# Kernel optimization log

Hardware: AMD Instinct MI355X
Metric: run time of the kernel (lower is better)

## Reference

```python
import jax, jax.numpy as jnp
import numpy as np

# Module hyper-parameters (match init_kwargs)
H = 8          # num_heads
F = 32         # attention_filters
HF = H * F     # 256, equals input channels C
RY, RX = 2, 2  # spatial_radius
PH, PW = 2 * RY + 1, 2 * RX + 1
S = PH * PW    # 25 neighbor offsets


def setup_inputs() -> dict:
    key = jax.random.key(0)
    ks = jax.random.split(key, 6)
    B, Y, X, C = 8, 128, 128, 256
    x = jax.random.normal(ks[0], (B, Y, X, C), dtype=jnp.float32)
    sc = 0.02
    Wq = jax.random.normal(ks[1], (C, HF), dtype=jnp.float32) * sc
    Wk = jax.random.normal(ks[2], (C, HF), dtype=jnp.float32) * sc
    Wv = jax.random.normal(ks[3], (C, HF), dtype=jnp.float32) * sc
    Wout = jax.random.normal(ks[4], (HF, C), dtype=jnp.float32) * sc
    pos_emb = jax.random.normal(ks[5], (S, HF), dtype=jnp.float32) * sc
    return {"x": x, "Wq": Wq, "Wk": Wk, "Wv": Wv, "Wout": Wout, "pos_emb": pos_emb}


def _centers(n, r):
    # clipped patch-center coordinate for each position
    c = jnp.arange(n)
    return jnp.clip(c, r, n - r - 1)


def reference(x, Wq, Wk, Wv, Wout, pos_emb):
    B, Y, X, C = x.shape
    dtype = x.dtype
    # 1x1 conv projections == channel matmuls
    Q = jnp.einsum('byxc,cf->byxf', x, Wq)
    K = jnp.einsum('byxc,cf->byxf', x, Wk)
    V = jnp.einsum('byxc,cf->byxf', x, Wv)

    # query spatial positional embedding (relative position to clipped center)
    yc = _centers(Y, RY)
    xc = _centers(X, RX)
    y_rel = jnp.arange(Y) - yc + RY          # [Y]
    x_rel = jnp.arange(X) - xc + RX          # [X]
    q_idx = y_rel[:, None] * PW + x_rel[None, :]  # [Y, X]
    Q = Q + pos_emb[q_idx]                   # [B,Y,X,HF]
    Q = Q.reshape(B, Y, X, H, F)

    scale = jnp.asarray(1.0 / np.sqrt(F), dtype)

    offsets = [(dy, dx) for dy in range(-RY, RY + 1) for dx in range(-RX, RX + 1)]

    # pass 1: per-offset scores (loop over fixed 25-neighborhood, rest vectorized)
    scores = []
    for s_idx, (dy, dx) in enumerate(offsets):
        ny = jnp.clip(yc + dy, 0, Y - 1)     # [Y]
        nx = jnp.clip(xc + dx, 0, X - 1)     # [X]
        Kn = K[:, ny][:, :, nx] + pos_emb[s_idx]        # [B,Y,X,HF]
        Kn = Kn.reshape(B, Y, X, H, F)
        scores.append(jnp.einsum('byxhf,byxhf->byxh', Q, Kn) * scale)
    scores = jnp.stack(scores, axis=-1)      # [B,Y,X,H,S]
    weights = jax.nn.softmax(scores, axis=-1)

    # pass 2: weighted value accumulation
    out_acc = jnp.zeros((B, Y, X, H, F), dtype=dtype)
    for s_idx, (dy, dx) in enumerate(offsets):
        ny = jnp.clip(yc + dy, 0, Y - 1)
        nx = jnp.clip(xc + dx, 0, X - 1)
        Vn = V[:, ny][:, :, nx].reshape(B, Y, X, H, F)
        out_acc = out_acc + weights[..., s_idx, None] * Vn

    out_acc = out_acc.reshape(B, Y, X, HF)
    out = jnp.einsum('byxf,fc->byxc', out_acc, Wout)
    return out
```

## Files before the change

### kernel.cpp

```cpp
#include <hip/hip_runtime.h>

#define DEVI __device__ __forceinline__

typedef short v8s __attribute__((ext_vector_type(8)));
typedef float v4f __attribute__((ext_vector_type(4)));
typedef _Float16 h2v __attribute__((ext_vector_type(2)));
typedef __fp16 fp16x2 __attribute__((ext_vector_type(2)));
typedef unsigned short u16;

typedef __attribute__((address_space(3))) unsigned int lds_u32;
typedef const __attribute__((address_space(1))) unsigned int glb_u32;

DEVI float bf2f(short s) {
  union { unsigned u; float f; } cv;
  cv.u = ((unsigned)(u16)s) << 16;
  return cv.f;
}
DEVI short f2bf(float f) {
  union { float f; unsigned u; } cv; cv.f = f;
  unsigned u = cv.u;
  return (short)((u + 0x7FFFu + ((u >> 16) & 1u)) >> 16);
}
DEVI unsigned cvtpk(float lo, float hi) {
  unsigned r;
  asm("v_cvt_pk_bf16_f32 %0, %1, %2" : "=v"(r) : "v"(lo), "v"(hi));
  return r;
}
DEVI unsigned pkh(float a, float b) {
  union { fp16x2 h; unsigned u; } cv;
  cv.h = __builtin_amdgcn_cvt_pkrtz(a, b);
  return cv.u;
}
DEVI float fdot2u(unsigned a, unsigned b, float c) {
  union { unsigned u; h2v h; } ca, cb; ca.u = a; cb.u = b;
  return __builtin_amdgcn_fdot2(ca.h, cb.h, c, false);
}
DEVI float h2lo(unsigned u) { union { unsigned u; h2v h; } c; c.u = u; return (float)c.h.x; }
DEVI float h2hi(unsigned u) { union { unsigned u; h2v h; } c; c.u = u; return (float)c.h.y; }
DEVI void gld16(const void* g, void* l) {
  __builtin_amdgcn_global_load_lds((glb_u32*)g, (lds_u32*)l, 16, 0, 0);
}

__global__ void prep_weights(const float* __restrict__ Wq, const float* __restrict__ Wk,
                             const float* __restrict__ Wv, const float* __restrict__ Wout,
                             short* __restrict__ WcT, short* __restrict__ WoT) {
  int n = blockIdx.x;
  int k = threadIdx.x;
  float v;
  if (n < 256)      v = Wq[k * 256 + n];
  else if (n < 512) v = Wk[k * 256 + (n - 256)];
  else              v = Wv[k * 256 + (n - 512)];
  WcT[n * 256 + k] = f2bf(v);
  if (n < 256) WoT[n * 256 + k] = f2bf(Wout[k * 256 + n]);
}

__global__ void x_cast(const float* __restrict__ x, short* __restrict__ xb) {
  for (size_t gidx = (size_t)blockIdx.x * 256 + threadIdx.x; gidx < 4194304;
       gidx += (size_t)4096 * 256) {
    const float4* src = reinterpret_cast<const float4*>(x + gidx * 8);
    float4 a = src[0], c = src[1];
    v8s pk;
    pk[0] = f2bf(a.x); pk[1] = f2bf(a.y); pk[2] = f2bf(a.z); pk[3] = f2bf(a.w);
    pk[4] = f2bf(c.x); pk[5] = f2bf(c.y); pk[6] = f2bf(c.z); pk[7] = f2bf(c.w);
    *reinterpret_cast<v8s*>(xb + gidx * 8) = pk;
  }
}

__launch_bounds__(512, 2)
__global__ void proj_gemm(const short* __restrict__ xb, const short* __restrict__ WcT,
                          const float* __restrict__ pos_emb,
                          short* __restrict__ Qb, short* __restrict__ Kb,
                          short* __restrict__ Vb) {
  __shared__ short As[2][256 * 64];
  __shared__ short Bs[2][256 * 64];
  const int t = threadIdx.x;
  const int bi = blockIdx.x;
  const int xcd = bi & 7;
  const int j = bi >> 3;
  const int mtl = j / 3, nt = j % 3;
  const int mt = xcd * 64 + mtl;
  const int m0 = mt * 256, n0 = nt * 256;
  const int wave = t >> 6, lane = t & 63;
  const int wm = (wave >> 2) * 128, wn = (wave & 3) * 64;
  const int lr = lane & 15, g = lane >> 4;

  const int ro = lane >> 3;
  const int colb = ((lane & 7) * 16) ^ (ro << 4);
  const char* aSrc0 = reinterpret_cast<const char*>(xb + (size_t)(m0 + ro) * 256) + colb;
  const char* bSrc0 = reinterpret_cast<const char*>(WcT + (size_t)(n0 + ro) * 256) + colb;

  auto stage = [&](int buf, int ks) {
#pragma unroll
    for (int c = 0; c < 4; ++c) {
      int cc = wave * 4 + c;
      gld16(aSrc0 + (size_t)cc * 8 * 512 + ks * 128, (char*)As[buf] + cc * 1024);
      gld16(bSrc0 + (size_t)cc * 8 * 512 + ks * 128, (char*)Bs[buf] + cc * 1024);
    }
  };

  v4f acc[8][4];
#pragma unroll
  for (int i = 0; i < 8; ++i)
#pragma unroll
    for (int jj = 0; jj < 4; ++jj) acc[i][jj] = (v4f){0.f, 0.f, 0.f, 0.f};

  stage(0, 0);
  __syncthreads();

#pragma unroll 1
  for (int s = 0; s < 4; ++s) {
    const int buf = s & 1;
    if (s < 3) stage(buf ^ 1, s + 1);

    const char* aB = (const char*)As[buf];
    const char* bB = (const char*)Bs[buf];
#pragma unroll
    for (int kk = 0; kk < 2; ++kk) {
      v8s bfr[4];
#pragma unroll
      for (int jj = 0; jj < 4; ++jj) {
        int rn = wn + jj * 16 + lr;
        bfr[jj] = *reinterpret_cast<const v8s*>(
            bB + ((rn * 128 + kk * 64 + g * 16) ^ ((rn & 7) << 4)));
      }
#pragma unroll
      for (int i = 0; i < 8; ++i) {
        int row = wm + i * 16 + lr;
        v8s af = *reinterpret_cast<const v8s*>(
            aB + ((row * 128 + kk * 64 + g * 16) ^ ((row & 7) << 4)));
#pragma unroll
        for (int jj = 0; jj < 4; ++jj)
          acc[i][jj] = __builtin_amdgcn_mfma_f32_16x16x32_bf16(bfr[jj], af, acc[i][jj], 0, 0, 0);
      }
    }
    __syncthreads();
  }

  short* dst = (nt == 0) ? Qb : (nt == 1) ? Kb : Vb;
#pragma unroll
  for (int i = 0; i < 8; ++i) {
    int p = m0 + wm + i * 16 + lr;
    int qi = 0;
    if (nt == 0) {
      int yy = (p >> 7) & 127, xx = p & 127;
      qi = (yy - min(max(yy, 2), 125) + 2) * 5 + (xx - min(max(xx, 2), 125) + 2);
    }
#pragma unroll
    for (int jj = 0; jj < 4; ++jj) {
      int nb = wn + jj * 16 + g * 4;
      v4f a = acc[i][jj];
      if (nt == 0) {
        float4 pe4 = *reinterpret_cast<const float4*>(pos_emb + qi * 256 + nb);
        a[0] += pe4.x; a[1] += pe4.y; a[2] += pe4.z; a[3] += pe4.w;
      }
      uint2 pk;
      if (nt == 2) {
        pk.x = cvtpk(a[0], a[1]);
        pk.y = cvtpk(a[2], a[3]);
      } else {
        pk.x = pkh(a[0], a[1]);
        pk.y = pkh(a[2], a[3]);
      }
      *reinterpret_cast<uint2*>(dst + (size_t)p * 256 + nb) = pk;
    }
  }
}

__launch_bounds__(256, 4)
__global__ void attn_kernel(const short* __restrict__ Qb, const short* __restrict__ Kb,
                            const short* __restrict__ Vb, const float* __restrict__ pos_emb,
                            short* __restrict__ ACC) {
  __shared__ float pe[25 * 256];
  for (int i = threadIdx.x; i < 1600; i += 256) {
    float4 vv = reinterpret_cast<const float4*>(pos_emb)[i];
    int w = i * 4;
    int f = w & 255;
    int dst = (w & ~255) + (f ^ ((f >> 5) << 2));
    *reinterpret_cast<float4*>(pe + dst) = vv;
  }

  const int t = threadIdx.x;
  const int half = t & 1, h = (t >> 1) & 7, pl = t >> 4;
  const int id = blockIdx.x;
  const int b = id & 7;
  const int local = id >> 3;
  const int bx = local & 31, by = local >> 5;
  const int xx = bx * 4 + (pl & 3);
  const int yy = by * 4 + (pl >> 2);
  const int yc = min(max(yy, 2), 125), xc = min(max(xx, 2), 125);
  const int fo = h * 32 + half * 16;
  const int hx4 = h << 2;
  const size_t pbase = ((size_t)((b * 128 + yy) * 128 + xx)) * 256 + fo;
  const size_t cbase = ((size_t)((b * 128 + yc) * 128 + xc)) * 256 + fo;
  const float SCALE2 = 0.17677669529663689f * 1.4426950408889634f;

  uint4 qA = *reinterpret_cast<const uint4*>(Qb + pbase);
  uint4 qB = *reinterpret_cast<const uint4*>(Qb + pbase + 8);
  float q[16];
  q[0] = h2lo(qA.x); q[1] = h2hi(qA.x); q[2] = h2lo(qA.y); q[3] = h2hi(qA.y);
  q[4] = h2lo(qA.z); q[5] = h2hi(qA.z); q[6] = h2lo(qA.w); q[7] = h2hi(qA.w);
  q[8] = h2lo(qB.x); q[9] = h2hi(qB.x); q[10] = h2lo(qB.y); q[11] = h2hi(qB.y);
  q[12] = h2lo(qB.z); q[13] = h2hi(qB.z); q[14] = h2lo(qB.w); q[15] = h2hi(qB.w);
  __syncthreads();

  float l = 0.f;
  float oa[16];
#pragma unroll
  for (int f = 0; f < 16; ++f) oa[f] = 0.f;

  const short* kb = Kb + cbase;
  const short* vb = Vb + cbase;
  const float* pb = pe + h * 32;
  const int j0 = (half * 16) ^ hx4;
  const int j1 = (half * 16 + 4) ^ hx4;
  const int j2 = (half * 16 + 8) ^ hx4;
  const int j3 = (half * 16 + 12) ^ hx4;

  uint4 kn0, kn1;
  v8s vn0, vn1;
  {
    const short* kp = kb + (-2 * 128 - 2) * 256;
    const short* vp = vb + (-2 * 128 - 2) * 256;
    kn0 = *reinterpret_cast<const uint4*>(kp);
    kn1 = *reinterpret_cast<const uint4*>(kp + 8);
    vn0 = *reinterpret_cast<const v8s*>(vp);
    vn1 = *reinterpret_cast<const v8s*>(vp + 8);
  }

#pragma unroll 1
  for (int dy = -2; dy <= 2; ++dy) {
    const float* prow = pb + ((dy + 2) * 5) * 256;
#pragma unroll 1
    for (int dx = -2; dx <= 2; ++dx) {
      uint4 k0 = kn0, k1 = kn1;
      v8s v0 = vn0, v1 = vn1;
      int ndx = dx + 1, ndy = dy;
      if (ndx > 2) { ndx = -2; ndy = dy + 1; }
      if (ndy <= 2) {
        const short* kp2 = kb + (ndy * 128 + ndx) * 256;
        const short* vp2 = vb + (ndy * 128 + ndx) * 256;
        kn0 = *reinterpret_cast<const uint4*>(kp2);
        kn1 = *reinterpret_cast<const uint4*>(kp2 + 8);
        vn0 = *reinterpret_cast<const v8s*>(vp2);
        vn1 = *reinterpret_cast<const v8s*>(vp2 + 8);
      }
      const float* pp = prow + (dx + 2) * 256;
      float4 p0 = *reinterpret_cast<const float4*>(pp + j0);
      float4 p1 = *reinterpret_cast<const float4*>(pp + j1);
      float4 p2 = *reinterpret_cast<const float4*>(pp + j2);
      float4 p3 = *reinterpret_cast<const float4*>(pp + j3);

      float d0 = 0.f, d1 = 0.f, d2 = 0.f, d3 = 0.f;
      d0 = fdot2u(qA.x, k0.x, d0); d1 = fdot2u(qA.y, k0.y, d1);
      d2 = fdot2u(qA.z, k0.z, d2); d3 = fdot2u(qA.w, k0.w, d3);
      d0 = fdot2u(qB.x, k1.x, d0); d1 = fdot2u(qB.y, k1.y, d1);
      d2 = fdot2u(qB.z, k1.z, d2); d3 = fdot2u(qB.w, k1.w, d3);

      d0 = fmaf(q[0], p0.x, d0); d0 = fmaf(q[1], p0.y, d0);
      d0 = fmaf(q[2], p0.z, d0); d0 = fmaf(q[3], p0.w, d0);
      d1 = fmaf(q[4], p1.x, d1); d1 = fmaf(q[5], p1.y, d1);
      d1 = fmaf(q[6], p1.z, d1); d1 = fmaf(q[7], p1.w, d1);
      d2 = fmaf(q[8], p2.x, d2); d2 = fmaf(q[9], p2.y, d2);
      d2 = fmaf(q[10], p2.z, d2); d2 = fmaf(q[11], p2.w, d2);
      d3 = fmaf(q[12], p3.x, d3); d3 = fmaf(q[13], p3.y, d3);
      d3 = fmaf(q[14], p3.z, d3); d3 = fmaf(q[15], p3.w, d3);

      float part = ((d0 + d1) + (d2 + d3)) * SCALE2;
      float full = part + __shfl_xor(part, 1);
      float w = exp2f(full);
      l += w;
#pragma unroll
      for (int e = 0; e < 8; ++e) oa[e] = fmaf(w, bf2f(v0[e]), oa[e]);
#pragma unroll
      for (int e = 0; e < 8; ++e) oa[8 + e] = fmaf(w, bf2f(v1[e]), oa[8 + e]);
    }
  }

  float inv = 1.f / l;
  uint4 o0, o1;
  o0.x = cvtpk(oa[0] * inv, oa[1] * inv);
  o0.y = cvtpk(oa[2] * inv, oa[3] * inv);
  o0.z = cvtpk(oa[4] * inv, oa[5] * inv);
  o0.w = cvtpk(oa[6] * inv, oa[7] * inv);
  o1.x = cvtpk(oa[8] * inv, oa[9] * inv);
  o1.y = cvtpk(oa[10] * inv, oa[11] * inv);
  o1.z = cvtpk(oa[12] * inv, oa[13] * inv);
  o1.w = cvtpk(oa[14] * inv, oa[15] * inv);
  *reinterpret_cast<uint4*>(ACC + pbase) = o0;
  *reinterpret_cast<uint4*>(ACC + pbase + 8) = o1;
}

__launch_bounds__(512, 2)
__global__ void out_gemm(const short* __restrict__ A, const short* __restrict__ WoT,
                         float* __restrict__ out) {
  __shared__ short As[2][256 * 64];
  __shared__ short Bs[2][256 * 64];
  const int t = threadIdx.x;
  const int bi = blockIdx.x;
  const int xcd = bi & 7;
  const int mt = xcd * 64 + (bi >> 3);
  const int m0 = mt * 256;
  const int wave = t >> 6, lane = t & 63;
  const int wm = (wave >> 2) * 128, wn = (wave & 3) * 64;
  const int lr = lane & 15, g = lane >> 4;

  const int ro = lane >> 3;
  const int colb = ((lane & 7) * 16) ^ (ro << 4);
  const char* aSrc0 = reinterpret_cast<const char*>(A + (size_t)(m0 + ro) * 256) + colb;
  const char* bSrc0 = reinterpret_cast<const char*>(WoT + (size_t)ro * 256) + colb;

  auto stage = [&](int buf, int ks) {
#pragma unroll
    for (int c = 0; c < 4; ++c) {
      int cc = wave * 4 + c;
      gld16(aSrc0 + (size_t)cc * 8 * 512 + ks * 128, (char*)As[buf] + cc * 1024);
      gld16(bSrc0 + (size_t)cc * 8 * 512 + ks * 128, (char*)Bs[buf] + cc * 1024);
    }
  };

  v4f acc[8][4];
#pragma unroll
  for (int i = 0; i < 8; ++i)
#pragma unroll
    for (int jj = 0; jj < 4; ++jj) acc[i][jj] = (v4f){0.f, 0.f, 0.f, 0.f};

  stage(0, 0);
  __syncthreads();

#pragma unroll 1
  for (int s = 0; s < 4; ++s) {
    const int buf = s & 1;
    if (s < 3) stage(buf ^ 1, s + 1);

    const char* aB = (const char*)As[buf];
    const char* bB = (const char*)Bs[buf];
#pragma unroll
    for (int kk = 0; kk < 2; ++kk) {
      v8s bfr[4];
#pragma unroll
      for (int jj = 0; jj < 4; ++jj) {
        int rn = wn + jj * 16 + lr;
        bfr[jj] = *reinterpret_cast<const v8s*>(
            bB + ((rn * 128 + kk * 64 + g * 16) ^ ((rn & 7) << 4)));
      }
#pragma unroll
      for (int i = 0; i < 8; ++i) {
        int row = wm + i * 16 + lr;
        v8s af = *reinterpret_cast<const v8s*>(
            aB + ((row * 128 + kk * 64 + g * 16) ^ ((row & 7) << 4)));
#pragma unroll
        for (int jj = 0; jj < 4; ++jj)
          acc[i][jj] = __builtin_amdgcn_mfma_f32_16x16x32_bf16(bfr[jj], af, acc[i][jj], 0, 0, 0);
      }
    }
    __syncthreads();
  }

#pragma unroll
  for (int i = 0; i < 8; ++i) {
    int p = m0 + wm + i * 16 + lr;
#pragma unroll
    for (int jj = 0; jj < 4; ++jj) {
      int nb = wn + jj * 16 + g * 4;
      float4 o;
      o.x = acc[i][jj][0]; o.y = acc[i][jj][1];
      o.z = acc[i][jj][2]; o.w = acc[i][jj][3];
      *reinterpret_cast<float4*>(out + (size_t)p * 256 + nb) = o;
    }
  }
}

extern "C" void kernel_launch(void* const* d_in, const int* in_sizes, int n_in,
                              void* d_out, int out_size, void* d_ws, size_t ws_size,
                              hipStream_t stream) {
  const float* x       = (const float*)d_in[0];
  const float* Wq      = (const float*)d_in[1];
  const float* Wk      = (const float*)d_in[2];
  const float* Wv      = (const float*)d_in[3];
  const float* Wout    = (const float*)d_in[4];
  const float* pos_emb = (const float*)d_in[5];
  float* out = (float*)d_out;

  char* ws = (char*)d_ws;
  short* WcT  = (short*)ws;
  short* WoT  = (short*)(ws + 393216);
  short* Qb   = (short*)(ws + 524288);
  short* Kb   = Qb + (size_t)131072 * 256;
  short* Vb   = Kb + (size_t)131072 * 256;
  short* ACCb = Vb + (size_t)131072 * 256;
  short* xb   = ACCb;

  prep_weights<<<768, 256, 0, stream>>>(Wq, Wk, Wv, Wout, WcT, WoT);
  x_cast<<<4096, 256, 0, stream>>>(x, xb);
  proj_gemm<<<1536, 512, 0, stream>>>(xb, WcT, pos_emb, Qb, Kb, Vb);
  attn_kernel<<<8192, 256, 0, stream>>>(Qb, Kb, Vb, pos_emb, ACCb);
  out_gemm<<<512, 512, 0, stream>>>(ACCb, WoT, out);
}
```

Baseline: 357.7 us.

## Rework attention kernel: fp16 V/pos-emb, packed half2 accumulation, one thread per head

```diff
diff --git a/kernel.cpp b/kernel.cpp
--- a/kernel.cpp
+++ b/kernel.cpp
@@ -1,4 +1,5 @@
 #include <hip/hip_runtime.h>
+#include <hip/hip_fp16.h>
 
 #define DEVI __device__ __forceinline__
 
@@ -35,8 +36,7 @@
   union { unsigned u; h2v h; } ca, cb; ca.u = a; cb.u = b;
   return __builtin_amdgcn_fdot2(ca.h, cb.h, c, false);
 }
-DEVI float h2lo(unsigned u) { union { unsigned u; h2v h; } c; c.u = u; return (float)c.h.x; }
-DEVI float h2hi(unsigned u) { union { unsigned u; h2v h; } c; c.u = u; return (float)c.h.y; }
+DEVI __half2 uh2(unsigned u) { union { unsigned u; __half2 h; } c; c.u = u; return c.h; }
 DEVI void gld16(const void* g, void* l) {
   __builtin_amdgcn_global_load_lds((glb_u32*)g, (lds_u32*)l, 16, 0, 0);
 }
@@ -154,140 +154,161 @@
         a[0] += pe4.x; a[1] += pe4.y; a[2] += pe4.z; a[3] += pe4.w;
       }
       uint2 pk;
-      if (nt == 2) {
-        pk.x = cvtpk(a[0], a[1]);
-        pk.y = cvtpk(a[2], a[3]);
-      } else {
-        pk.x = pkh(a[0], a[1]);
-        pk.y = pkh(a[2], a[3]);
-      }
+      pk.x = pkh(a[0], a[1]);
+      pk.y = pkh(a[2], a[3]);
       *reinterpret_cast<uint2*>(dst + (size_t)p * 256 + nb) = pk;
     }
   }
 }
 
-__launch_bounds__(256, 4)
+__launch_bounds__(256, 2)
 __global__ void attn_kernel(const short* __restrict__ Qb, const short* __restrict__ Kb,
                             const short* __restrict__ Vb, const float* __restrict__ pos_emb,
                             short* __restrict__ ACC) {
-  __shared__ float pe[25 * 256];
+  __shared__ __align__(16) unsigned pe16[25 * 128];
   for (int i = threadIdx.x; i < 1600; i += 256) {
     float4 vv = reinterpret_cast<const float4*>(pos_emb)[i];
-    int w = i * 4;
-    int f = w & 255;
-    int dst = (w & ~255) + (f ^ ((f >> 5) << 2));
-    *reinterpret_cast<float4*>(pe + dst) = vv;
+    int s = i >> 6;
+    int jw = (i & 63) * 2;
+    int swz = (jw & ~15) | ((((jw >> 2) ^ (jw >> 5)) & 3) << 2) | (jw & 3);
+    uint2 pk2;
+    pk2.x = pkh(vv.x, vv.y);
+    pk2.y = pkh(vv.z, vv.w);
+    *reinterpret_cast<uint2*>(pe16 + s * 128 + swz) = pk2;
   }
 
   const int t = threadIdx.x;
-  const int half = t & 1, h = (t >> 1) & 7, pl = t >> 4;
+  const int h = t & 7, pl = t >> 3;
   const int id = blockIdx.x;
   const int b = id & 7;
   const int local = id >> 3;
   const int bx = local & 31, by = local >> 5;
   const int xx = bx * 4 + (pl & 3);
-  const int yy = by * 4 + (pl >> 2);
+  const int yy = by * 8 + (pl >> 2);
   const int yc = min(max(yy, 2), 125), xc = min(max(xx, 2), 125);
-  const int fo = h * 32 + half * 16;
-  const int hx4 = h << 2;
+  const int fo = h * 32;
   const size_t pbase = ((size_t)((b * 128 + yy) * 128 + xx)) * 256 + fo;
   const size_t cbase = ((size_t)((b * 128 + yc) * 128 + xc)) * 256 + fo;
   const float SCALE2 = 0.17677669529663689f * 1.4426950408889634f;
 
-  uint4 qA = *reinterpret_cast<const uint4*>(Qb + pbase);
-  uint4 qB = *reinterpret_cast<const uint4*>(Qb + pbase + 8);
-  float q[16];
-  q[0] = h2lo(qA.x); q[1] = h2hi(qA.x); q[2] = h2lo(qA.y); q[3] = h2hi(qA.y);
-  q[4] = h2lo(qA.z); q[5] = h2hi(qA.z); q[6] = h2lo(qA.w); q[7] = h2hi(qA.w);
-  q[8] = h2lo(qB.x); q[9] = h2hi(qB.x); q[10] = h2lo(qB.y); q[11] = h2hi(qB.y);
-  q[12] = h2lo(qB.z); q[13] = h2hi(qB.z); q[14] = h2lo(qB.w); q[15] = h2hi(qB.w);
+  uint4 q0 = *reinterpret_cast<const uint4*>(Qb + pbase);
+  uint4 q1 = *reinterpret_cast<const uint4*>(Qb + pbase + 8);
+  uint4 q2 = *reinterpret_cast<const uint4*>(Qb + pbase + 16);
+  uint4 q3 = *reinterpret_cast<const uint4*>(Qb + pbase + 24);
   __syncthreads();
 
+  const unsigned* peb = pe16 + h * 16;
+  const int hs = (h >> 1) & 3;
+  const int r0 = ((0 ^ hs) & 3) * 4;
+  const int r1 = ((1 ^ hs) & 3) * 4;
+  const int r2 = ((2 ^ hs) & 3) * 4;
+  const int r3 = ((3 ^ hs) & 3) * 4;
+
   float l = 0.f;
-  float oa[16];
-#pragma unroll
-  for (int f = 0; f < 16; ++f) oa[f] = 0.f;
+  __half2 oa[16];
+#pragma unroll
+  for (int j = 0; j < 16; ++j) oa[j] = uh2(0u);
 
   const short* kb = Kb + cbase;
   const short* vb = Vb + cbase;
-  const float* pb = pe + h * 32;
-  const int j0 = (half * 16) ^ hx4;
-  const int j1 = (half * 16 + 4) ^ hx4;
-  const int j2 = (half * 16 + 8) ^ hx4;
-  const int j3 = (half * 16 + 12) ^ hx4;
-
-  uint4 kn0, kn1;
-  v8s vn0, vn1;
-  {
-    const short* kp = kb + (-2 * 128 - 2) * 256;
-    const short* vp = vb + (-2 * 128 - 2) * 256;
-    kn0 = *reinterpret_cast<const uint4*>(kp);
-    kn1 = *reinterpret_cast<const uint4*>(kp + 8);
-    vn0 = *reinterpret_cast<const v8s*>(vp);
-    vn1 = *reinterpret_cast<const v8s*>(vp + 8);
-  }
 
 #pragma unroll 1
   for (int dy = -2; dy <= 2; ++dy) {
-    const float* prow = pb + ((dy + 2) * 5) * 256;
-#pragma unroll 1
-    for (int dx = -2; dx <= 2; ++dx) {
-      uint4 k0 = kn0, k1 = kn1;
-      v8s v0 = vn0, v1 = vn1;
-      int ndx = dx + 1, ndy = dy;
-      if (ndx > 2) { ndx = -2; ndy = dy + 1; }
-      if (ndy <= 2) {
-        const short* kp2 = kb + (ndy * 128 + ndx) * 256;
-        const short* vp2 = vb + (ndy * 128 + ndx) * 256;
-        kn0 = *reinterpret_cast<const uint4*>(kp2);
-        kn1 = *reinterpret_cast<const uint4*>(kp2 + 8);
-        vn0 = *reinterpret_cast<const v8s*>(vp2);
-        vn1 = *reinterpret_cast<const v8s*>(vp2 + 8);
-      }
-      const float* pp = prow + (dx + 2) * 256;
-      float4 p0 = *reinterpret_cast<const float4*>(pp + j0);
-      float4 p1 = *reinterpret_cast<const float4*>(pp + j1);
-      float4 p2 = *reinterpret_cast<const float4*>(pp + j2);
-      float4 p3 = *reinterpret_cast<const float4*>(pp + j3);
+    const short* krow = kb + dy * (128 * 256);
+    const short* vrow = vb + dy * (128 * 256);
+    const unsigned* perow = peb + ((dy + 2) * 5) * 128;
+#pragma unroll
+    for (int dxi = 0; dxi < 5; ++dxi) {
+      const short* kp = krow + (dxi - 2) * 256;
+      const short* vp = vrow + (dxi - 2) * 256;
+      uint4 k0 = *reinterpret_cast<const uint4*>(kp);
+      uint4 k1 = *reinterpret_cast<const uint4*>(kp + 8);
+      uint4 k2 = *reinterpret_cast<const uint4*>(kp + 16);
+      uint4 k3 = *reinterpret_cast<const uint4*>(kp + 24);
+      uint4 v0 = *reinterpret_cast<const uint4*>(vp);
+      uint4 v1 = *reinterpret_cast<const uint4*>(vp + 8);
+      uint4 v2 = *reinterpret_cast<const uint4*>(vp + 16);
+      uint4 v3 = *reinterpret_cast<const uint4*>(vp + 24);
+      const unsigned* ps = perow + dxi * 128;
+      uint4 p0 = *reinterpret_cast<const uint4*>(ps + r0);
+      uint4 p1 = *reinterpret_cast<const uint4*>(ps + r1);
+      uint4 p2 = *reinterpret_cast<const uint4*>(ps + r2);
+      uint4 p3 = *reinterpret_cast<const uint4*>(ps + r3);
 
       float d0 = 0.f, d1 = 0.f, d2 = 0.f, d3 = 0.f;
-      d0 = fdot2u(qA.x, k0.x, d0); d1 = fdot2u(qA.y, k0.y, d1);
-      d2 = fdot2u(qA.z, k0.z, d2); d3 = fdot2u(qA.w, k0.w, d3);
-      d0 = fdot2u(qB.x, k1.x, d0); d1 = fdot2u(qB.y, k1.y, d1);
-      d2 = fdot2u(qB.z, k1.z, d2); d3 = fdot2u(qB.w, k1.w, d3);
-
-      d0 = fmaf(q[0], p0.x, d0); d0 = fmaf(q[1], p0.y, d0);
-      d0 = fmaf(q[2], p0.z, d0); d0 = fmaf(q[3], p0.w, d0);
-      d1 = fmaf(q[4], p1.x, d1); d1 = fmaf(q[5], p1.y, d1);
-      d1 = fmaf(q[6], p1.z, d1); d1 = fmaf(q[7], p1.w, d1);
-      d2 = fmaf(q[8], p2.x, d2); d2 = fmaf(q[9], p2.y, d2);
-      d2 = fmaf(q[10], p2.z, d2); d2 = fmaf(q[11], p2.w, d2);
-      d3 = fmaf(q[12], p3.x, d3); d3 = fmaf(q[13], p3.y, d3);
-      d3 = fmaf(q[14], p3.z, d3); d3 = fmaf(q[15], p3.w, d3);
-
-      float part = ((d0 + d1) + (d2 + d3)) * SCALE2;
-      float full = part + __shfl_xor(part, 1);
-      float w = exp2f(full);
+      d0 = fdot2u(q0.x, k0.x, d0); d1 = fdot2u(q0.y, k0.y, d1);
+      d2 = fdot2u(q0.z, k0.z, d2); d3 = fdot2u(q0.w, k0.w, d3);
+      d0 = fdot2u(q1.x, k1.x, d0); d1 = fdot2u(q1.y, k1.y, d1);
+      d2 = fdot2u(q1.z, k1.z, d2); d3 = fdot2u(q1.w, k1.w, d3);
+      d0 = fdot2u(q2.x, k2.x, d0); d1 = fdot2u(q2.y, k2.y, d1);
+      d2 = fdot2u(q2.z, k2.z, d2); d3 = fdot2u(q2.w, k2.w, d3);
+      d0 = fdot2u(q3.x, k3.x, d0); d1 = fdot2u(q3.y, k3.y, d1);
+      d2 = fdot2u(q3.z, k3.z, d2); d3 = fdot2u(q3.w, k3.w, d3);
+      d0 = fdot2u(q0.x, p0.x, d0); d1 = fdot2u(q0.y, p0.y, d1);
+      d2 = fdot2u(q0.z, p0.z, d2); d3 = fdot2u(q0.w, p0.w, d3);
+      d0 = fdot2u(q1.x, p1.x, d0); d1 = fdot2u(q1.y, p1.y, d1);
+      d2 = fdot2u(q1.z, p1.z, d2); d3 = fdot2u(q1.w, p1.w, d3);
+      d0 = fdot2u(q2.x, p2.x, d0); d1 = fdot2u(q2.y, p2.y, d1);
+      d2 = fdot2u(q2.z, p2.z, d2); d3 = fdot2u(q2.w, p2.w, d3);
+      d0 = fdot2u(q3.x, p3.x, d0); d1 = fdot2u(q3.y, p3.y, d1);
+      d2 = fdot2u(q3.z, p3.z, d2); d3 = fdot2u(q3.w, p3.w, d3);
+
+      float sc = ((d0 + d1) + (d2 + d3)) * SCALE2;
+      float w = exp2f(sc);
       l += w;
-#pragma unroll
-      for (int e = 0; e < 8; ++e) oa[e] = fmaf(w, bf2f(v0[e]), oa[e]);
-#pragma unroll
-      for (int e = 0; e < 8; ++e) oa[8 + e] = fmaf(w, bf2f(v1[e]), oa[8 + e]);
+      __half2 w2 = uh2(pkh(w, w));
+      oa[0]  = __hfma2(w2, uh2(v0.x), oa[0]);
+      oa[1]  = __hfma2(w2, uh2(v0.y), oa[1]);
+      oa[2]  = __hfma2(w2, uh2(v0.z), oa[2]);
+      oa[3]  = __hfma2(w2, uh2(v0.w), oa[3]);
+      oa[4]  = __hfma2(w2, uh2(v1.x), oa[4]);
+      oa[5]  = __hfma2(w2, uh2(v1.y), oa[5]);
+      oa[6]  = __hfma2(w2, uh2(v1.z), oa[6]);
+      oa[7]  = __hfma2(w2, uh2(v1.w), oa[7]);
+      oa[8]  = __hfma2(w2, uh2(v2.x), oa[8]);
+      oa[9]  = __hfma2(w2, uh2(v2.y), oa[9]);
+      oa[10] = __hfma2(w2, uh2(v2.z), oa[10]);
+      oa[11] = __hfma2(w2, uh2(v2.w), oa[11]);
+      oa[12] = __hfma2(w2, uh2(v3.x), oa[12]);
+      oa[13] = __hfma2(w2, uh2(v3.y), oa[13]);
+      oa[14] = __hfma2(w2, uh2(v3.z), oa[14]);
+      oa[15] = __hfma2(w2, uh2(v3.w), oa[15]);
     }
   }
 
   float inv = 1.f / l;
-  uint4 o0, o1;
-  o0.x = cvtpk(oa[0] * inv, oa[1] * inv);
-  o0.y = cvtpk(oa[2] * inv, oa[3] * inv);
-  o0.z = cvtpk(oa[4] * inv, oa[5] * inv);
-  o0.w = cvtpk(oa[6] * inv, oa[7] * inv);
-  o1.x = cvtpk(oa[8] * inv, oa[9] * inv);
-  o1.y = cvtpk(oa[10] * inv, oa[11] * inv);
-  o1.z = cvtpk(oa[12] * inv, oa[13] * inv);
-  o1.w = cvtpk(oa[14] * inv, oa[15] * inv);
-  *reinterpret_cast<uint4*>(ACC + pbase) = o0;
-  *reinterpret_cast<uint4*>(ACC + pbase + 8) = o1;
+  unsigned ow[8];
+#pragma unroll
+  for (int j = 0; j < 8; ++j) {
+    float a0 = __low2float(oa[2 * j]) * inv;
+    float a1 = __high2float(oa[2 * j]) * inv;
+    float a2 = __low2float(oa[2 * j + 1]) * inv;
+    float a3 = __high2float(oa[2 * j + 1]) * inv;
+    (void)a2; (void)a3;
+    ow[j] = 0;
+  }
+  uint4 s0, s1;
+  s0.x = cvtpk(__low2float(oa[0]) * inv, __high2float(oa[0]) * inv);
+  s0.y = cvtpk(__low2float(oa[1]) * inv, __high2float(oa[1]) * inv);
+  s0.z = cvtpk(__low2float(oa[2]) * inv, __high2float(oa[2]) * inv);
+  s0.w = cvtpk(__low2float(oa[3]) * inv, __high2float(oa[3]) * inv);
+  s1.x = cvtpk(__low2float(oa[4]) * inv, __high2float(oa[4]) * inv);
+  s1.y = cvtpk(__low2float(oa[5]) * inv, __high2float(oa[5]) * inv);
+  s1.z = cvtpk(__low2float(oa[6]) * inv, __high2float(oa[6]) * inv);
+  s1.w = cvtpk(__low2float(oa[7]) * inv, __high2float(oa[7]) * inv);
+  *reinterpret_cast<uint4*>(ACC + pbase) = s0;
+  *reinterpret_cast<uint4*>(ACC + pbase + 8) = s1;
+  uint4 s2, s3;
+  s2.x = cvtpk(__low2float(oa[8]) * inv, __high2float(oa[8]) * inv);
+  s2.y = cvtpk(__low2float(oa[9]) * inv, __high2float(oa[9]) * inv);
+  s2.z = cvtpk(__low2float(oa[10]) * inv, __high2float(oa[10]) * inv);
+  s2.w = cvtpk(__low2float(oa[11]) * inv, __high2float(oa[11]) * inv);
+  s3.x = cvtpk(__low2float(oa[12]) * inv, __high2float(oa[12]) * inv);
+  s3.y = cvtpk(__low2float(oa[13]) * inv, __high2float(oa[13]) * inv);
+  s3.z = cvtpk(__low2float(oa[14]) * inv, __high2float(oa[14]) * inv);
+  s3.w = cvtpk(__low2float(oa[15]) * inv, __high2float(oa[15]) * inv);
+  *reinterpret_cast<uint4*>(ACC + pbase + 16) = s2;
+  *reinterpret_cast<uint4*>(ACC + pbase + 24) = s3;
 }
 
 __launch_bounds__(512, 2)
@@ -393,6 +414,6 @@
   prep_weights<<<768, 256, 0, stream>>>(Wq, Wk, Wv, Wout, WcT, WoT);
   x_cast<<<4096, 256, 0, stream>>>(x, xb);
   proj_gemm<<<1536, 512, 0, stream>>>(xb, WcT, pos_emb, Qb, Kb, Vb);
-  attn_kernel<<<8192, 256, 0, stream>>>(Qb, Kb, Vb, pos_emb, ACCb);
+  attn_kernel<<<4096, 256, 0, stream>>>(Qb, Kb, Vb, pos_emb, ACCb);
   out_gemm<<<512, 512, 0, stream>>>(ACCb, WoT, out);
 }
```

Result: slower. 579.3 us (+62.0%).
